# Kernel tuning notes

Measured on AMD Instinct MI355X. Metric: run time of the kernel, lower is better.

Reference implementation:

```python
import jax, jax.numpy as jnp
import numpy as np

N_ENT = 100000
N_REL = 1000
RANK = 256
B = 1024
MAX_NB = 50


def setup_inputs() -> dict:
    key = jax.random.key(0)
    ks = jax.random.split(key, 12)
    s = 0.001  # init_size scaling as in the torch module
    x = jax.random.randint(ks[0], (B, 3), 0, N_REL)  # in-range for ents and rels
    nb_idx = jax.random.randint(ks[1], (B, MAX_NB), 0, N_ENT)
    lhs_w = jax.random.normal(ks[2], (N_ENT, RANK), jnp.float32) * s
    rel_w = jax.random.normal(ks[3], (N_REL, RANK), jnp.float32) * s
    rhs_w = jax.random.normal(ks[4], (N_ENT, RANK), jnp.float32) * s
    W_w = jax.random.normal(ks[5], (RANK, 2 * RANK), jnp.float32) * 0.05
    W_b = jnp.zeros((RANK,), jnp.float32)
    W2_w = jax.random.normal(ks[6], (RANK, RANK), jnp.float32) * 0.05
    W2_b = jnp.zeros((RANK,), jnp.float32)
    Wo_w = jax.random.normal(ks[7], (1, RANK), jnp.float32) * 0.05
    Wo_b = jnp.zeros((1,), jnp.float32)
    Uo_w = jax.random.normal(ks[8], (1, RANK), jnp.float32) * 0.05
    Uo_b = jnp.zeros((1,), jnp.float32)
    return dict(x=x, nb_idx=nb_idx, lhs_w=lhs_w, rel_w=rel_w, rhs_w=rhs_w,
                W_w=W_w, W_b=W_b, W2_w=W2_w, W2_b=W2_b,
                Wo_w=Wo_w, Wo_b=Wo_b, Uo_w=Uo_w, Uo_b=Uo_b)


def reference(x, nb_idx, lhs_w, rel_w, rhs_w, W_w, W_b, W2_w, W2_b, Wo_w, Wo_b, Uo_w, Uo_b):
    lhs = lhs_w[x[:, 0]]            # [B, r]
    rel = rel_w[x[:, 1]]            # [B, r]
    rhs = rhs_w[x[:, 2]]            # [B, r]
    trp_E = jnp.concatenate([lhs, rel], axis=1)          # [B, 2r]
    w = trp_E @ W_w.T + W_b                               # [B, r]
    nb_E = rhs_w[nb_idx]                                  # [B, M, r] irregular gather
    alpha = jax.nn.softmax(jnp.einsum('bk,bmk->bm', w, nb_E), axis=1)
    e_c = jnp.einsum('bm,bmk->bk', alpha, nb_E) @ W2_w.T + W2_b  # [B, r]
    g = jax.nn.sigmoid((lhs * rel) @ Uo_w.T + Uo_b + e_c @ Wo_w.T + Wo_b)  # [B, 1]
    gated_e_c = g * e_c + (1.0 - g)                       # [B, r]
    tot_forward = (lhs * rel * gated_e_c) @ rhs_w.T       # [B, n_ent]
    return tot_forward, (lhs, rel, rhs, e_c)
```

## Files before the change

kernel.cpp:

```cpp
#include <hip/hip_runtime.h>
#include <hip/hip_bf16.h>

#define B_TRIPLES 1024
#define N_ENT 100000
#define RANK 256
#define MAX_NB 50

typedef float f32x4 __attribute__((ext_vector_type(4)));
typedef __bf16 bf16x8 __attribute__((ext_vector_type(8)));

__device__ __forceinline__ unsigned short f32_to_bf16_bits(float f) {
    unsigned u = __float_as_uint(f);
    unsigned r = ((u >> 16) & 1u) + 0x7fffu;
    return (unsigned short)((u + r) >> 16);
}

__global__ __launch_bounds__(256) void triple_kernel(
    const int* __restrict__ x, const int* __restrict__ nb_idx,
    const float* __restrict__ lhs_w, const float* __restrict__ rel_w,
    const float* __restrict__ rhs_w,
    const float* __restrict__ W_w, const float* __restrict__ W_b,
    const float* __restrict__ W2_w, const float* __restrict__ W2_b,
    const float* __restrict__ Wo_w, const float* __restrict__ Wo_b,
    const float* __restrict__ Uo_w, const float* __restrict__ Uo_b,
    float* __restrict__ out_tail, unsigned short* __restrict__ qb)
{
    __shared__ float trp[2 * RANK];
    __shared__ float nb_s[MAX_NB * RANK];
    __shared__ float w_s[RANK];
    __shared__ float alpha_s[MAX_NB];
    __shared__ int   nbrow[MAX_NB];
    __shared__ float red[8];

    const int b    = blockIdx.x;
    const int k    = threadIdx.x;
    const int lane = k & 63;
    const int wv   = k >> 6;

    const int i0 = x[b * 3 + 0];
    const int i1 = x[b * 3 + 1];
    const int i2 = x[b * 3 + 2];

    const float lhs  = lhs_w[(size_t)i0 * RANK + k];
    const float rel  = rel_w[(size_t)i1 * RANK + k];
    const float rhsv = rhs_w[(size_t)i2 * RANK + k];

    out_tail[0 * B_TRIPLES * RANK + b * RANK + k] = lhs;
    out_tail[1 * B_TRIPLES * RANK + b * RANK + k] = rel;
    out_tail[2 * B_TRIPLES * RANK + b * RANK + k] = rhsv;

    trp[k]        = lhs;
    trp[RANK + k] = rel;
    if (k < MAX_NB) nbrow[k] = nb_idx[b * MAX_NB + k];
    __syncthreads();

    for (int m = 0; m < MAX_NB; ++m)
        nb_s[m * RANK + k] = rhs_w[(size_t)nbrow[m] * RANK + k];

    float acc = W_b[k];
    const float4* Wr = (const float4*)(W_w + (size_t)k * (2 * RANK));
    #pragma unroll 8
    for (int j = 0; j < (2 * RANK) / 4; ++j) {
        float4 w4 = Wr[j];
        acc += w4.x * trp[4 * j + 0] + w4.y * trp[4 * j + 1]
             + w4.z * trp[4 * j + 2] + w4.w * trp[4 * j + 3];
    }
    w_s[k] = acc;
    __syncthreads();

    for (int m = wv; m < MAX_NB; m += 4) {
        float p = 0.f;
        #pragma unroll
        for (int t = 0; t < 4; ++t) {
            int kk = lane + 64 * t;
            p += w_s[kk] * nb_s[m * RANK + kk];
        }
        #pragma unroll
        for (int off = 32; off > 0; off >>= 1) p += __shfl_down(p, off);
        if (lane == 0) alpha_s[m] = p;
    }
    __syncthreads();

    if (wv == 0) {
        float v = (lane < MAX_NB) ? alpha_s[lane] : -1e30f;
        float mx = v;
        #pragma unroll
        for (int off = 1; off < 64; off <<= 1) mx = fmaxf(mx, __shfl_xor(mx, off));
        float e = (lane < MAX_NB) ? __expf(v - mx) : 0.f;
        float s = e;
        #pragma unroll
        for (int off = 1; off < 64; off <<= 1) s += __shfl_xor(s, off);
        if (lane < MAX_NB) alpha_s[lane] = e / s;
    }
    __syncthreads();

    float ecp = 0.f;
    for (int m = 0; m < MAX_NB; ++m) ecp += alpha_s[m] * nb_s[m * RANK + k];
    __syncthreads();
    trp[k] = ecp;
    __syncthreads();

    float ec = W2_b[k];
    const float4* W2r = (const float4*)(W2_w + (size_t)k * RANK);
    #pragma unroll 8
    for (int j = 0; j < RANK / 4; ++j) {
        float4 w4 = W2r[j];
        ec += w4.x * trp[4 * j + 0] + w4.y * trp[4 * j + 1]
            + w4.z * trp[4 * j + 2] + w4.w * trp[4 * j + 3];
    }
    out_tail[3 * B_TRIPLES * RANK + b * RANK + k] = ec;

    float part = lhs * rel * Uo_w[k] + ec * Wo_w[k];
    #pragma unroll
    for (int off = 32; off > 0; off >>= 1) part += __shfl_down(part, off);
    if (lane == 0) red[wv] = part;
    __syncthreads();
    if (k == 0) {
        float s = red[0] + red[1] + red[2] + red[3] + Uo_b[0] + Wo_b[0];
        red[4] = 1.f / (1.f + __expf(-s));
    }
    __syncthreads();
    const float g = red[4];
    const float gated = g * ec + (1.f - g);
    qb[b * RANK + k] = f32_to_bf16_bits(lhs * rel * gated);
}

__global__ __launch_bounds__(256) void cvt_kernel(
    const float* __restrict__ in, unsigned short* __restrict__ outp)
{
    size_t t = (size_t)blockIdx.x * 256 + threadIdx.x;
    const float4* p = (const float4*)in + 2 * t;
    float4 a = p[0], c = p[1];
    uint4 o;
    o.x = (unsigned)f32_to_bf16_bits(a.x) | ((unsigned)f32_to_bf16_bits(a.y) << 16);
    o.y = (unsigned)f32_to_bf16_bits(a.z) | ((unsigned)f32_to_bf16_bits(a.w) << 16);
    o.z = (unsigned)f32_to_bf16_bits(c.x) | ((unsigned)f32_to_bf16_bits(c.y) << 16);
    o.w = (unsigned)f32_to_bf16_bits(c.z) | ((unsigned)f32_to_bf16_bits(c.w) << 16);
    ((uint4*)outp)[t] = o;
}

__global__ __launch_bounds__(512) void gemm_kernel(
    const unsigned short* __restrict__ rhsb,
    const unsigned short* __restrict__ qb,
    float* __restrict__ out)
{
    const int lane = threadIdx.x & 63;
    const int wv   = threadIdx.x >> 6;
    const int r    = lane & 15;
    const int quad = lane >> 4;

    const int e_blk  = blockIdx.x * 64;
    const int b_base = blockIdx.y * 512 + wv * 64;

    f32x4 acc[4][4] = {};

    #pragma unroll
    for (int kt = 0; kt < 8; ++kt) {
        const int ko = kt * 32 + quad * 8;
        union { uint4 u; bf16x8 v; } a[4], bb[4];
        #pragma unroll
        for (int tm = 0; tm < 4; ++tm) {
            const int brow = b_base + tm * 16 + r;
            a[tm].u = *(const uint4*)(qb + (size_t)brow * RANK + ko);
        }
        #pragma unroll
        for (int tn = 0; tn < 4; ++tn) {
            int e = e_blk + tn * 16 + r;
            if (e >= N_ENT) e = N_ENT - 1;
            bb[tn].u = *(const uint4*)(rhsb + (size_t)e * RANK + ko);
        }
        #pragma unroll
        for (int tm = 0; tm < 4; ++tm)
            #pragma unroll
            for (int tn = 0; tn < 4; ++tn)
                acc[tm][tn] = __builtin_amdgcn_mfma_f32_16x16x32_bf16(
                    a[tm].v, bb[tn].v, acc[tm][tn], 0, 0, 0);
    }

    #pragma unroll
    for (int tm = 0; tm < 4; ++tm) {
        #pragma unroll
        for (int i = 0; i < 4; ++i) {
            const int brow = b_base + tm * 16 + quad * 4 + i;
            float* orow = out + (size_t)brow * N_ENT;
            #pragma unroll
            for (int tn = 0; tn < 4; ++tn) {
                const int e = e_blk + tn * 16 + r;
                if (e < N_ENT) orow[e] = acc[tm][tn][i];
            }
        }
    }
}

extern "C" void kernel_launch(void* const* d_in, const int* in_sizes, int n_in,
                              void* d_out, int out_size, void* d_ws, size_t ws_size,
                              hipStream_t stream)
{
    const int*   x     = (const int*)d_in[0];
    const int*   nb    = (const int*)d_in[1];
    const float* lhs_w = (const float*)d_in[2];
    const float* rel_w = (const float*)d_in[3];
    const float* rhs_w = (const float*)d_in[4];
    const float* W_w   = (const float*)d_in[5];
    const float* W_b   = (const float*)d_in[6];
    const float* W2_w  = (const float*)d_in[7];
    const float* W2_b  = (const float*)d_in[8];
    const float* Wo_w  = (const float*)d_in[9];
    const float* Wo_b  = (const float*)d_in[10];
    const float* Uo_w  = (const float*)d_in[11];
    const float* Uo_b  = (const float*)d_in[12];

    float* out      = (float*)d_out;
    float* out_tail = out + (size_t)B_TRIPLES * N_ENT;

    unsigned short* rhsb = (unsigned short*)d_ws;
    unsigned short* qb   = rhsb + (size_t)N_ENT * RANK;

    triple_kernel<<<B_TRIPLES, 256, 0, stream>>>(
        x, nb, lhs_w, rel_w, rhs_w, W_w, W_b, W2_w, W2_b,
        Wo_w, Wo_b, Uo_w, Uo_b, out_tail, qb);

    cvt_kernel<<<12500, 256, 0, stream>>>(rhs_w, rhsb);

    gemm_kernel<<<dim3(1563, 2), 512, 0, stream>>>(rhsb, qb, out);

    (void)in_sizes; (void)n_in; (void)out_size; (void)ws_size;
}
```

Measured before the change: 790.7 us.

## Transpose weights for coalesced loads, drop neighbor LDS staging, swizzle GEMM blocks by XCD

A new prep kernel transposes W and W2 into a float4-interleaved layout, so each thread's weight loads in the triple kernel coalesce across the wavefront instead of striding by whole rows. The 50KB neighbor staging buffer in shared memory is removed and neighbor rows are read directly from global memory in both the score and weighted-sum passes, which cuts LDS use and should raise occupancy. The GEMM grid becomes 1D and is remapped so that consecutive blocks on the same XCD share entity tiles, improving L2 reuse of the rhs matrix. In exchange there is an extra kernel launch and neighbor rows are read from global memory twice.

```diff
diff --git a/kernel.cpp b/kernel.cpp
--- a/kernel.cpp
+++ b/kernel.cpp
@@ -15,18 +15,32 @@
     return (unsigned short)((u + r) >> 16);
 }
 
+__global__ __launch_bounds__(256) void prep_kernel(
+    const float* __restrict__ W_w, const float* __restrict__ W2_w,
+    float* __restrict__ Wt4, float* __restrict__ W2t4)
+{
+    int t = blockIdx.x * 256 + threadIdx.x;
+    if (t < RANK * 2 * RANK) {
+        int k = t >> 9, j = t & 511;
+        Wt4[((j >> 2) * RANK + k) * 4 + (j & 3)] = W_w[t];
+    } else {
+        int u = t - RANK * 2 * RANK;
+        int k = u >> 8, j = u & 255;
+        W2t4[((j >> 2) * RANK + k) * 4 + (j & 3)] = W2_w[u];
+    }
+}
+
 __global__ __launch_bounds__(256) void triple_kernel(
     const int* __restrict__ x, const int* __restrict__ nb_idx,
     const float* __restrict__ lhs_w, const float* __restrict__ rel_w,
     const float* __restrict__ rhs_w,
-    const float* __restrict__ W_w, const float* __restrict__ W_b,
-    const float* __restrict__ W2_w, const float* __restrict__ W2_b,
+    const float* __restrict__ Wt4, const float* __restrict__ W_b,
+    const float* __restrict__ W2t4, const float* __restrict__ W2_b,
     const float* __restrict__ Wo_w, const float* __restrict__ Wo_b,
     const float* __restrict__ Uo_w, const float* __restrict__ Uo_b,
     float* __restrict__ out_tail, unsigned short* __restrict__ qb)
 {
     __shared__ float trp[2 * RANK];
-    __shared__ float nb_s[MAX_NB * RANK];
     __shared__ float w_s[RANK];
     __shared__ float alpha_s[MAX_NB];
     __shared__ int   nbrow[MAX_NB];
@@ -54,27 +68,24 @@
     if (k < MAX_NB) nbrow[k] = nb_idx[b * MAX_NB + k];
     __syncthreads();
 
-    for (int m = 0; m < MAX_NB; ++m)
-        nb_s[m * RANK + k] = rhs_w[(size_t)nbrow[m] * RANK + k];
-
     float acc = W_b[k];
-    const float4* Wr = (const float4*)(W_w + (size_t)k * (2 * RANK));
-    #pragma unroll 8
-    for (int j = 0; j < (2 * RANK) / 4; ++j) {
-        float4 w4 = Wr[j];
-        acc += w4.x * trp[4 * j + 0] + w4.y * trp[4 * j + 1]
-             + w4.z * trp[4 * j + 2] + w4.w * trp[4 * j + 3];
+    {
+        const float4* Wp = (const float4*)Wt4;
+        #pragma unroll 8
+        for (int jc = 0; jc < (2 * RANK) / 4; ++jc) {
+            float4 wv4 = Wp[jc * RANK + k];
+            float4 t   = *(const float4*)&trp[jc * 4];
+            acc += wv4.x * t.x + wv4.y * t.y + wv4.z * t.z + wv4.w * t.w;
+        }
     }
     w_s[k] = acc;
     __syncthreads();
 
     for (int m = wv; m < MAX_NB; m += 4) {
-        float p = 0.f;
-        #pragma unroll
-        for (int t = 0; t < 4; ++t) {
-            int kk = lane + 64 * t;
-            p += w_s[kk] * nb_s[m * RANK + kk];
-        }
+        const float* nrow = rhs_w + (size_t)nbrow[m] * RANK;
+        float4 nv  = *(const float4*)(nrow + lane * 4);
+        float4 wv4 = *(const float4*)(w_s + lane * 4);
+        float p = nv.x * wv4.x + nv.y * wv4.y + nv.z * wv4.z + nv.w * wv4.w;
         #pragma unroll
         for (int off = 32; off > 0; off >>= 1) p += __shfl_down(p, off);
         if (lane == 0) alpha_s[m] = p;
@@ -95,18 +106,21 @@
     __syncthreads();
 
     float ecp = 0.f;
-    for (int m = 0; m < MAX_NB; ++m) ecp += alpha_s[m] * nb_s[m * RANK + k];
-    __syncthreads();
+    #pragma unroll 5
+    for (int m = 0; m < MAX_NB; ++m)
+        ecp += alpha_s[m] * rhs_w[(size_t)nbrow[m] * RANK + k];
     trp[k] = ecp;
     __syncthreads();
 
     float ec = W2_b[k];
-    const float4* W2r = (const float4*)(W2_w + (size_t)k * RANK);
-    #pragma unroll 8
-    for (int j = 0; j < RANK / 4; ++j) {
-        float4 w4 = W2r[j];
-        ec += w4.x * trp[4 * j + 0] + w4.y * trp[4 * j + 1]
-            + w4.z * trp[4 * j + 2] + w4.w * trp[4 * j + 3];
+    {
+        const float4* W2p = (const float4*)W2t4;
+        #pragma unroll 8
+        for (int jc = 0; jc < RANK / 4; ++jc) {
+            float4 wv4 = W2p[jc * RANK + k];
+            float4 t   = *(const float4*)&trp[jc * 4];
+            ec += wv4.x * t.x + wv4.y * t.y + wv4.z * t.z + wv4.w * t.w;
+        }
     }
     out_tail[3 * B_TRIPLES * RANK + b * RANK + k] = ec;
 
@@ -149,8 +163,13 @@
     const int r    = lane & 15;
     const int quad = lane >> 4;
 
-    const int e_blk  = blockIdx.x * 64;
-    const int b_base = blockIdx.y * 512 + wv * 64;
+    const int bid = blockIdx.x;
+    constexpr int Q = 390, R = 6;
+    const int xcd = bid & 7, off = bid >> 3;
+    const int swz = (xcd < R ? xcd * (Q + 1) : R * (Q + 1) + (xcd - R) * Q) + off;
+
+    const int e_blk  = (swz >> 1) * 64;
+    const int b_base = (swz & 1) * 512 + wv * 64;
 
     f32x4 acc[4][4] = {};
 
@@ -215,14 +234,18 @@
 
     unsigned short* rhsb = (unsigned short*)d_ws;
     unsigned short* qb   = rhsb + (size_t)N_ENT * RANK;
+    float* Wt4  = (float*)(qb + (size_t)B_TRIPLES * RANK);
+    float* W2t4 = Wt4 + (size_t)(2 * RANK) * RANK;
+
+    prep_kernel<<<768, 256, 0, stream>>>(W_w, W2_w, Wt4, W2t4);
 
     triple_kernel<<<B_TRIPLES, 256, 0, stream>>>(
-        x, nb, lhs_w, rel_w, rhs_w, W_w, W_b, W2_w, W2_b,
+        x, nb, lhs_w, rel_w, rhs_w, Wt4, W_b, W2t4, W2_b,
         Wo_w, Wo_b, Uo_w, Uo_b, out_tail, qb);
 
     cvt_kernel<<<12500, 256, 0, stream>>>(rhs_w, rhsb);
 
-    gemm_kernel<<<dim3(1563, 2), 512, 0, stream>>>(rhsb, qb, out);
+    gemm_kernel<<<3126, 512, 0, stream>>>(rhsb, qb, out);
 
     (void)in_sizes; (void)n_in; (void)out_size; (void)ws_size;
 }
```

New measurement: 748.3 us. 5.4% less time.
